# Performance work log

Measured on AMD Instinct MI355X. Metric: run time of the kernel, lower is better.

Reference implementation:

```python
import jax, jax.numpy as jnp
import numpy as np

TEMPERATURE = 0.07
EPS = 1e-8  # torch CosineSimilarity eps


def setup_inputs() -> dict:
    key = jax.random.key(0)
    k1, k2, k3 = jax.random.split(key, 3)
    N, D = 8192, 512
    features = jax.random.normal(k1, (N, D), dtype=jnp.float32)
    positive_mask = jax.random.randint(k2, (N, N), 0, 2, dtype=jnp.int32)
    negative_mask = jax.random.randint(k3, (N, N), 0, 2, dtype=jnp.int32)
    return {"features": features, "positive_mask": positive_mask, "negative_mask": negative_mask}


def reference(features, positive_mask, negative_mask):
    N = positive_mask.shape[0]
    self_contrast = 1.0 - jnp.eye(N, dtype=features.dtype)  # zero diagonal
    pos = positive_mask.astype(features.dtype) * self_contrast  # [N, N]
    neg = negative_mask.astype(features.dtype) * self_contrast  # [N, N]

    # cosine similarity via normalized matmul (same math as broadcasted CosineSimilarity)
    norm = jnp.maximum(jnp.linalg.norm(features, axis=1, keepdims=True), EPS)
    fn = features / norm  # [N, D]
    sim = jnp.matmul(fn, fn.T) / TEMPERATURE  # [N, N]

    logits_max = jax.lax.stop_gradient(jnp.max(sim, axis=1, keepdims=True))
    e = jnp.exp(sim - logits_max)  # [N, N]

    positives = e * pos
    log_neg_sum = jnp.log(jnp.sum(e * neg, axis=1, keepdims=True))  # [N, 1]
    log_prob = positives - log_neg_sum  # [N, N] (faithful to source: exp-masked, not log)

    cardinal = jnp.sum(pos, axis=1)
    cardinal = jnp.where(cardinal == 0, 1.0, cardinal)
    log_prob_sum = jnp.sum(log_prob * pos, axis=1)
    loss = -log_prob_sum / cardinal
    return jnp.mean(loss)
```

## Files before the change

kernel.cpp:

```cpp
#include <hip/hip_runtime.h>
#include <hip/hip_bf16.h>
#include <math.h>

#define NN 8192
#define DD 512
#define INV_T 14.285714285714286f

typedef __attribute__((ext_vector_type(8))) short s16x8;
typedef __attribute__((ext_vector_type(4))) float f32x4;

__device__ __forceinline__ unsigned short f32_to_bf16(float f) {
  unsigned int u = __float_as_uint(f);
  u += 0x7FFFu + ((u >> 16) & 1u);
  return (unsigned short)(u >> 16);
}

__device__ __forceinline__ void async16(const void* g, void* l) {
  __builtin_amdgcn_global_load_lds((__attribute__((address_space(1))) void*)(void*)g,
                                   (__attribute__((address_space(3))) void*)l,
                                   16, 0, 0);
}

__global__ __launch_bounds__(256) void normalize_kernel(const float* __restrict__ f,
                                                        unsigned short* __restrict__ fnb) {
  const int wave = threadIdx.x >> 6;
  const int lane = threadIdx.x & 63;
  const int row  = blockIdx.x * 4 + wave;
  const float* src = f + (size_t)row * DD + lane * 8;
  float4 v0 = *(const float4*)src;
  float4 v1 = *(const float4*)(src + 4);
  float ss = v0.x*v0.x + v0.y*v0.y + v0.z*v0.z + v0.w*v0.w
           + v1.x*v1.x + v1.y*v1.y + v1.z*v1.z + v1.w*v1.w;
  #pragma unroll
  for (int o = 32; o; o >>= 1) ss += __shfl_xor(ss, o);
  const float r = 1.0f / fmaxf(sqrtf(ss), 1e-8f);
  ushort4 a, b;
  a.x = f32_to_bf16(v0.x * r); a.y = f32_to_bf16(v0.y * r);
  a.z = f32_to_bf16(v0.z * r); a.w = f32_to_bf16(v0.w * r);
  b.x = f32_to_bf16(v1.x * r); b.y = f32_to_bf16(v1.y * r);
  b.z = f32_to_bf16(v1.z * r); b.w = f32_to_bf16(v1.w * r);
  unsigned short* dst = fnb + (size_t)row * DD + lane * 8;
  *(ushort4*)dst = a;
  *(ushort4*)(dst + 4) = b;
}

__global__ __launch_bounds__(256) void fused_kernel(const unsigned short* __restrict__ fnb,
                                                    const int* __restrict__ posm,
                                                    const int* __restrict__ negm,
                                                    float* __restrict__ Spos,
                                                    float* __restrict__ Sneg,
                                                    float* __restrict__ Pcnt) {
  const int bid = blockIdx.x;
  int bi = (int)(64.5 - sqrt(64.5 * 64.5 - 2.0 * (double)bid));
  while (64 * bi - bi * (bi - 1) / 2 > bid) --bi;
  while (64 * (bi + 1) - (bi + 1) * bi / 2 <= bid) ++bi;
  const int bj = bi + (bid - (64 * bi - bi * (bi - 1) / 2));
  const int I = bi * 128;
  const int J = bj * 128;
  const bool offdiag = (bi != bj);

  const int tid  = threadIdx.x;
  const int wave = tid >> 6;
  const int lane = tid & 63;
  const int wm = wave >> 1;
  const int wn = wave & 1;
  const int q   = lane >> 4;
  const int c16 = lane & 15;

  __shared__ alignas(16) unsigned short lA[128 * 32];
  __shared__ alignas(16) unsigned short lB[128 * 32];
  __shared__ alignas(16) unsigned long long mdir[2][128][2];
  __shared__ alignas(16) unsigned long long mtr [2][128][2];

  {
    const int tile = wave >> 1;
    const int msel = wave & 1;
    const int R0 = tile ? J : I;
    const int C0 = tile ? I : J;
    const int* mb = msel ? negm : posm;
    unsigned long long (*dst)[2] = tile ? mtr[msel] : mdir[msel];
    if (!(tile && !offdiag)) {
      for (int k = 0; k < 128; k += 8) {
        int v[16];
        #pragma unroll
        for (int u = 0; u < 16; ++u)
          v[u] = __builtin_nontemporal_load(
              mb + (size_t)(R0 + k + (u >> 1)) * NN + C0 + (u & 1) * 64 + lane);
        unsigned long long b[16];
        #pragma unroll
        for (int u = 0; u < 16; ++u) b[u] = __ballot(v[u] != 0);
        if (lane == 0) {
          #pragma unroll
          for (int u = 0; u < 16; u += 2) {
            ulonglong2 t; t.x = b[u]; t.y = b[u + 1];
            *(ulonglong2*)&dst[k + (u >> 1)][0] = t;
          }
        }
      }
    }
  }

  f32x4 acc[4][4];
  const f32x4 z4 = {0.f, 0.f, 0.f, 0.f};
  #pragma unroll
  for (int mt = 0; mt < 4; ++mt)
    #pragma unroll
    for (int nt = 0; nt < 4; ++nt) acc[mt][nt] = z4;

  for (int kk = 0; kk < DD / 32; ++kk) {
    const int k0 = kk * 32;
    #pragma unroll
    for (int c = 0; c < 2; ++c) {
      const int fidx = tid + c * 256;
      const int row  = fidx >> 2;
      const int p    = fidx & 3;
      const int csrc = (p ^ ((row >> 1) & 3)) & 3;
      async16(fnb + (size_t)(I + row) * DD + k0 + csrc * 8, (char*)lA + fidx * 16);
      async16(fnb + (size_t)(J + row) * DD + k0 + csrc * 8, (char*)lB + fidx * 16);
    }
    __syncthreads();

    s16x8 aF[4], bF[4];
    #pragma unroll
    for (int t = 0; t < 4; ++t) {
      const int arow = wm * 64 + t * 16 + c16;
      const int apos = (q ^ ((arow >> 1) & 3)) & 3;
      aF[t] = *(const s16x8*)((const char*)lA + arow * 64 + apos * 16);
      const int brow = wn * 64 + t * 16 + c16;
      const int bpos = (q ^ ((brow >> 1) & 3)) & 3;
      bF[t] = *(const s16x8*)((const char*)lB + brow * 64 + bpos * 16);
    }
    #pragma unroll
    for (int mt = 0; mt < 4; ++mt)
      #pragma unroll
      for (int nt = 0; nt < 4; ++nt)
        acc[mt][nt] = __builtin_amdgcn_mfma_f32_16x16x32_bf16(aF[mt], bF[nt], acc[mt][nt], 0, 0, 0);
    __syncthreads();
  }

  const bool hasdiag = (bi == bj) && (wm == wn);

  unsigned long long pT[4], nT[4];
  if (offdiag) {
    #pragma unroll
    for (int nt = 0; nt < 4; ++nt) {
      const int cl = wn * 64 + nt * 16 + c16;
      pT[nt] = mtr[0][cl][wm];
      nT[nt] = mtr[1][cl][wm];
    }
  }
  float tsp[4] = {0,0,0,0}, tsn[4] = {0,0,0,0};

  #pragma unroll
  for (int mt = 0; mt < 4; ++mt) {
    const int rl = wm * 64 + mt * 16 + q * 4;
    const int rbase = I + rl;
    unsigned long long pw[4], nw[4];
    #pragma unroll
    for (int r = 0; r < 4; ++r) {
      pw[r] = mdir[0][rl + r][wn];
      nw[r] = mdir[1][rl + r][wn];
      if (hasdiag) {
        const unsigned long long m = ~(1ULL << (mt * 16 + q * 4 + r));
        pw[r] &= m;
        nw[r] &= m;
      }
    }
    float dsp[4] = {0,0,0,0}, dsn[4] = {0,0,0,0};
    #pragma unroll
    for (int nt = 0; nt < 4; ++nt) {
      float e[4];
      #pragma unroll
      for (int r = 0; r < 4; ++r)
        e[r] = __expf(acc[mt][nt][r] * INV_T - INV_T);
      const int bpos = nt * 16 + c16;
      #pragma unroll
      for (int r = 0; r < 4; ++r) {
        const float pf = (float)((pw[r] >> bpos) & 1ULL);
        const float nf = (float)((nw[r] >> bpos) & 1ULL);
        dsp[r] = fmaf(e[r], pf, dsp[r]);
        dsn[r] = fmaf(e[r], nf, dsn[r]);
      }
      if (offdiag) {
        const int bt = mt * 16 + q * 4;
        #pragma unroll
        for (int r = 0; r < 4; ++r) {
          tsp[nt] = fmaf(e[r], (float)((pT[nt] >> (bt + r)) & 1ULL), tsp[nt]);
          tsn[nt] = fmaf(e[r], (float)((nT[nt] >> (bt + r)) & 1ULL), tsn[nt]);
        }
      }
    }
    #pragma unroll
    for (int r = 0; r < 4; ++r) {
      float a = dsp[r], b = dsn[r];
      #pragma unroll
      for (int o = 1; o <= 8; o <<= 1) {
        a += __shfl_xor(a, o);
        b += __shfl_xor(b, o);
      }
      if (c16 == 0) {
        atomicAdd(&Spos[rbase + r], a);
        atomicAdd(&Sneg[rbase + r], b);
        atomicAdd(&Pcnt[rbase + r], (float)__popcll(pw[r]));
      }
    }
  }

  if (offdiag) {
    #pragma unroll
    for (int nt = 0; nt < 4; ++nt) {
      float a = tsp[nt], b = tsn[nt];
      a += __shfl_xor(a, 16); a += __shfl_xor(a, 32);
      b += __shfl_xor(b, 16); b += __shfl_xor(b, 32);
      if (q == 0) {
        const int col = J + wn * 64 + nt * 16 + c16;
        atomicAdd(&Spos[col], a);
        atomicAdd(&Sneg[col], b);
        atomicAdd(&Pcnt[col], (float)__popcll(pT[nt]));
      }
    }
  }
}

__global__ __launch_bounds__(256) void finalize_kernel(const float* __restrict__ Spos,
                                                       const float* __restrict__ Sneg,
                                                       const float* __restrict__ Pcnt,
                                                       float* __restrict__ out) {
  float local = 0.f;
  for (int i = threadIdx.x; i < NN; i += 256) {
    const float sp = Spos[i], sn = Sneg[i], pc = Pcnt[i];
    const float card = (pc == 0.f) ? 1.f : pc;
    local += (logf(sn) * pc - sp) / card;
  }
  #pragma unroll
  for (int o = 32; o; o >>= 1) local += __shfl_xor(local, o);
  __shared__ float red[4];
  if ((threadIdx.x & 63) == 0) red[threadIdx.x >> 6] = local;
  __syncthreads();
  if (threadIdx.x == 0)
    out[0] = (red[0] + red[1] + red[2] + red[3]) * (1.0f / (float)NN);
}

extern "C" void kernel_launch(void* const* d_in, const int* in_sizes, int n_in,
                              void* d_out, int out_size, void* d_ws, size_t ws_size,
                              hipStream_t stream) {
  const float* feat = (const float*)d_in[0];
  const int* posm   = (const int*)d_in[1];
  const int* negm   = (const int*)d_in[2];
  float* out = (float*)d_out;

  char* ws = (char*)d_ws;
  unsigned short* fnb = (unsigned short*)ws;
  float* Spos = (float*)(ws + (size_t)8 * 1024 * 1024);
  float* Sneg = Spos + NN;
  float* Pcnt = Sneg + NN;

  hipMemsetAsync(Spos, 0, 3 * NN * sizeof(float), stream);
  normalize_kernel<<<NN / 4, 256, 0, stream>>>(feat, fnb);
  fused_kernel<<<2080, 256, 0, stream>>>(fnb, posm, negm, Spos, Sneg, Pcnt);
  finalize_kernel<<<1, 256, 0, stream>>>(Spos, Sneg, Pcnt, out);
}
```

Measured before the change: 654.4 us.

## Load MFMA operands directly from global, vectorize mask loads, raise occupancy

```diff
diff --git a/kernel.cpp b/kernel.cpp
--- a/kernel.cpp
+++ b/kernel.cpp
@@ -8,17 +8,13 @@
 
 typedef __attribute__((ext_vector_type(8))) short s16x8;
 typedef __attribute__((ext_vector_type(4))) float f32x4;
+typedef __attribute__((ext_vector_type(4))) int   i32x4;
+typedef __attribute__((ext_vector_type(4))) unsigned int u32x4;
 
 __device__ __forceinline__ unsigned short f32_to_bf16(float f) {
   unsigned int u = __float_as_uint(f);
   u += 0x7FFFu + ((u >> 16) & 1u);
   return (unsigned short)(u >> 16);
-}
-
-__device__ __forceinline__ void async16(const void* g, void* l) {
-  __builtin_amdgcn_global_load_lds((__attribute__((address_space(1))) void*)(void*)g,
-                                   (__attribute__((address_space(3))) void*)l,
-                                   16, 0, 0);
 }
 
 __global__ __launch_bounds__(256) void normalize_kernel(const float* __restrict__ f,
@@ -44,12 +40,12 @@
   *(ushort4*)(dst + 4) = b;
 }
 
-__global__ __launch_bounds__(256) void fused_kernel(const unsigned short* __restrict__ fnb,
-                                                    const int* __restrict__ posm,
-                                                    const int* __restrict__ negm,
-                                                    float* __restrict__ Spos,
-                                                    float* __restrict__ Sneg,
-                                                    float* __restrict__ Pcnt) {
+__global__ __launch_bounds__(256, 3) void fused_kernel(const unsigned short* __restrict__ fnb,
+                                                       const int* __restrict__ posm,
+                                                       const int* __restrict__ negm,
+                                                       float* __restrict__ Spos,
+                                                       float* __restrict__ Sneg,
+                                                       float* __restrict__ Pcnt) {
   const int bid = blockIdx.x;
   int bi = (int)(64.5 - sqrt(64.5 * 64.5 - 2.0 * (double)bid));
   while (64 * bi - bi * (bi - 1) / 2 > bid) --bi;
@@ -67,10 +63,8 @@
   const int q   = lane >> 4;
   const int c16 = lane & 15;
 
-  __shared__ alignas(16) unsigned short lA[128 * 32];
-  __shared__ alignas(16) unsigned short lB[128 * 32];
-  __shared__ alignas(16) unsigned long long mdir[2][128][2];
-  __shared__ alignas(16) unsigned long long mtr [2][128][2];
+  __shared__ unsigned int bdir[2][128][4];
+  __shared__ unsigned int btr [2][128][4];
 
   {
     const int tile = wave >> 1;
@@ -78,22 +72,32 @@
     const int R0 = tile ? J : I;
     const int C0 = tile ? I : J;
     const int* mb = msel ? negm : posm;
-    unsigned long long (*dst)[2] = tile ? mtr[msel] : mdir[msel];
+    unsigned int (*dst)[4] = tile ? btr[msel] : bdir[msel];
+    const int sub  = lane >> 5;
+    const int col4 = (lane & 31) * 4;
     if (!(tile && !offdiag)) {
-      for (int k = 0; k < 128; k += 8) {
-        int v[16];
+      for (int i = 0; i < 64; i += 4) {
+        i32x4 v[4];
         #pragma unroll
-        for (int u = 0; u < 16; ++u)
+        for (int u = 0; u < 4; ++u) {
+          const int row = (i + u) * 2 + sub;
           v[u] = __builtin_nontemporal_load(
-              mb + (size_t)(R0 + k + (u >> 1)) * NN + C0 + (u & 1) * 64 + lane);
-        unsigned long long b[16];
+                   (const i32x4*)(mb + (size_t)(R0 + row) * NN + C0 + col4));
+        }
         #pragma unroll
-        for (int u = 0; u < 16; ++u) b[u] = __ballot(v[u] != 0);
-        if (lane == 0) {
-          #pragma unroll
-          for (int u = 0; u < 16; u += 2) {
-            ulonglong2 t; t.x = b[u]; t.y = b[u + 1];
-            *(ulonglong2*)&dst[k + (u >> 1)][0] = t;
+        for (int u = 0; u < 4; ++u) {
+          const unsigned long long b0 = __ballot(v[u].x != 0);
+          const unsigned long long b1 = __ballot(v[u].y != 0);
+          const unsigned long long b2 = __ballot(v[u].z != 0);
+          const unsigned long long b3 = __ballot(v[u].w != 0);
+          if (lane < 2) {
+            const int sh = lane * 32;
+            u32x4 w;
+            w.x = (unsigned int)(b0 >> sh);
+            w.y = (unsigned int)(b1 >> sh);
+            w.z = (unsigned int)(b2 >> sh);
+            w.w = (unsigned int)(b3 >> sh);
+            *(u32x4*)&dst[(i + u) * 2 + lane][0] = w;
           }
         }
       }
@@ -107,101 +111,106 @@
     #pragma unroll
     for (int nt = 0; nt < 4; ++nt) acc[mt][nt] = z4;
 
+  const unsigned short* aP[4];
+  const unsigned short* bP[4];
+  #pragma unroll
+  for (int t = 0; t < 4; ++t) {
+    aP[t] = fnb + (size_t)(I + wm * 64 + t * 16 + c16) * DD + q * 8;
+    bP[t] = fnb + (size_t)(J + wn * 64 + t * 16 + c16) * DD + q * 8;
+  }
+  s16x8 aF[2][4], bF[2][4];
+  #pragma unroll
+  for (int t = 0; t < 4; ++t) {
+    aF[0][t] = *(const s16x8*)aP[t];
+    bF[0][t] = *(const s16x8*)bP[t];
+  }
+  #pragma unroll 2
   for (int kk = 0; kk < DD / 32; ++kk) {
-    const int k0 = kk * 32;
-    #pragma unroll
-    for (int c = 0; c < 2; ++c) {
-      const int fidx = tid + c * 256;
-      const int row  = fidx >> 2;
-      const int p    = fidx & 3;
-      const int csrc = (p ^ ((row >> 1) & 3)) & 3;
-      async16(fnb + (size_t)(I + row) * DD + k0 + csrc * 8, (char*)lA + fidx * 16);
-      async16(fnb + (size_t)(J + row) * DD + k0 + csrc * 8, (char*)lB + fidx * 16);
-    }
-    __syncthreads();
-
-    s16x8 aF[4], bF[4];
-    #pragma unroll
-    for (int t = 0; t < 4; ++t) {
-      const int arow = wm * 64 + t * 16 + c16;
-      const int apos = (q ^ ((arow >> 1) & 3)) & 3;
-      aF[t] = *(const s16x8*)((const char*)lA + arow * 64 + apos * 16);
-      const int brow = wn * 64 + t * 16 + c16;
-      const int bpos = (q ^ ((brow >> 1) & 3)) & 3;
-      bF[t] = *(const s16x8*)((const char*)lB + brow * 64 + bpos * 16);
+    const int cur = kk & 1, nxt = cur ^ 1;
+    if (kk < DD / 32 - 1) {
+      const int off = (kk + 1) * 32;
+      #pragma unroll
+      for (int t = 0; t < 4; ++t) {
+        aF[nxt][t] = *(const s16x8*)(aP[t] + off);
+        bF[nxt][t] = *(const s16x8*)(bP[t] + off);
+      }
     }
     #pragma unroll
     for (int mt = 0; mt < 4; ++mt)
       #pragma unroll
       for (int nt = 0; nt < 4; ++nt)
-        acc[mt][nt] = __builtin_amdgcn_mfma_f32_16x16x32_bf16(aF[mt], bF[nt], acc[mt][nt], 0, 0, 0);
-    __syncthreads();
-  }
+        acc[mt][nt] = __builtin_amdgcn_mfma_f32_16x16x32_bf16(aF[cur][mt], bF[cur][nt], acc[mt][nt], 0, 0, 0);
+  }
+
+  __syncthreads();
 
   const bool hasdiag = (bi == bj) && (wm == wn);
 
-  unsigned long long pT[4], nT[4];
+  u32x4 pT4[4], nT4[4];
   if (offdiag) {
     #pragma unroll
     for (int nt = 0; nt < 4; ++nt) {
       const int cl = wn * 64 + nt * 16 + c16;
-      pT[nt] = mtr[0][cl][wm];
-      nT[nt] = mtr[1][cl][wm];
+      pT4[nt] = *(const u32x4*)&btr[0][cl][0];
+      nT4[nt] = *(const u32x4*)&btr[1][cl][0];
     }
   }
   float tsp[4] = {0,0,0,0}, tsn[4] = {0,0,0,0};
+  const int jword = c16 & 3;
+  const int cshift = c16 >> 2;
 
   #pragma unroll
   for (int mt = 0; mt < 4; ++mt) {
     const int rl = wm * 64 + mt * 16 + q * 4;
-    const int rbase = I + rl;
-    unsigned long long pw[4], nw[4];
+    unsigned int pwv[4], nwv[4];
     #pragma unroll
     for (int r = 0; r < 4; ++r) {
-      pw[r] = mdir[0][rl + r][wn];
-      nw[r] = mdir[1][rl + r][wn];
-      if (hasdiag) {
-        const unsigned long long m = ~(1ULL << (mt * 16 + q * 4 + r));
-        pw[r] &= m;
-        nw[r] &= m;
-      }
-    }
-    float dsp[4] = {0,0,0,0}, dsn[4] = {0,0,0,0};
+      pwv[r] = bdir[0][rl + r][jword];
+      nwv[r] = bdir[1][rl + r][jword];
+    }
+    float dsp[4] = {0,0,0,0}, dsn[4] = {0,0,0,0}, dpc[4] = {0,0,0,0};
     #pragma unroll
     for (int nt = 0; nt < 4; ++nt) {
       float e[4];
       #pragma unroll
       for (int r = 0; r < 4; ++r)
         e[r] = __expf(acc[mt][nt][r] * INV_T - INV_T);
-      const int bpos = nt * 16 + c16;
+      const int cbit = wn * 16 + nt * 4 + cshift;
+      const int cl   = wn * 64 + nt * 16 + c16;
       #pragma unroll
       for (int r = 0; r < 4; ++r) {
-        const float pf = (float)((pw[r] >> bpos) & 1ULL);
-        const float nf = (float)((nw[r] >> bpos) & 1ULL);
+        float pf = (float)((pwv[r] >> cbit) & 1u);
+        float nf = (float)((nwv[r] >> cbit) & 1u);
+        if (hasdiag && (rl + r == cl)) { pf = 0.f; nf = 0.f; }
         dsp[r] = fmaf(e[r], pf, dsp[r]);
         dsn[r] = fmaf(e[r], nf, dsn[r]);
+        dpc[r] += pf;
       }
       if (offdiag) {
-        const int bt = mt * 16 + q * 4;
+        const int tc = wm * 16 + mt * 4 + q;
+        const unsigned int* pw = (const unsigned int*)&pT4[nt];
+        const unsigned int* nw = (const unsigned int*)&nT4[nt];
         #pragma unroll
         for (int r = 0; r < 4; ++r) {
-          tsp[nt] = fmaf(e[r], (float)((pT[nt] >> (bt + r)) & 1ULL), tsp[nt]);
-          tsn[nt] = fmaf(e[r], (float)((nT[nt] >> (bt + r)) & 1ULL), tsn[nt]);
+          tsp[nt] = fmaf(e[r], (float)((pw[r] >> tc) & 1u), tsp[nt]);
+          tsn[nt] = fmaf(e[r], (float)((nw[r] >> tc) & 1u), tsn[nt]);
         }
       }
     }
     #pragma unroll
     for (int r = 0; r < 4; ++r) {
-      float a = dsp[r], b = dsn[r];
+      float a = dsp[r], b = dsn[r], p = dpc[r];
       #pragma unroll
       for (int o = 1; o <= 8; o <<= 1) {
         a += __shfl_xor(a, o);
         b += __shfl_xor(b, o);
+        p += __shfl_xor(p, o);
       }
       if (c16 == 0) {
-        atomicAdd(&Spos[rbase + r], a);
-        atomicAdd(&Sneg[rbase + r], b);
-        atomicAdd(&Pcnt[rbase + r], (float)__popcll(pw[r]));
+        const int row = I + rl + r;
+        atomicAdd(&Spos[row], a);
+        atomicAdd(&Sneg[row], b);
+        atomicAdd(&Pcnt[row], p);
       }
     }
   }
@@ -212,11 +221,15 @@
       float a = tsp[nt], b = tsn[nt];
       a += __shfl_xor(a, 16); a += __shfl_xor(a, 32);
       b += __shfl_xor(b, 16); b += __shfl_xor(b, 32);
+      const int col = J + wn * 64 + nt * 16 + c16;
       if (q == 0) {
-        const int col = J + wn * 64 + nt * 16 + c16;
         atomicAdd(&Spos[col], a);
         atomicAdd(&Sneg[col], b);
-        atomicAdd(&Pcnt[col], (float)__popcll(pT[nt]));
+      }
+      if (q == 0 && wm == 0) {
+        const unsigned int* pw = (const unsigned int*)&pT4[nt];
+        const float pc = (float)(__popc(pw[0]) + __popc(pw[1]) + __popc(pw[2]) + __popc(pw[3]));
+        atomicAdd(&Pcnt[col], pc);
       }
     }
   }
```

After: 658.3 us. Within noise of the previous version (+0.6%).
